# Kernel optimization log

Measured on AMD Instinct MI355X. Metric: run time of the kernel, lower is better.

The kernel has to match this reference:

```python
import jax, jax.numpy as jnp
import numpy as np

PRE_NMS_TOPK = 6000
POST_NMS_TOPK = 1000
NMS_THRESH = 0.7
MIN_SIZE = 16.0
NEG = -1e9  # stand-in for -inf that is safe under autodiff


def setup_inputs() -> dict:
    key = jax.random.key(0)
    k1, k2, k3, k4, k5, k6, k7, k8 = jax.random.split(key, 8)
    B, A = 8, 200000
    N = B * A
    # realistic anchors: centers within a ~1333x800 canvas, sizes 16..256
    cx = jax.random.uniform(k1, (N,), minval=0.0, maxval=1200.0)
    cy = jax.random.uniform(k2, (N,), minval=0.0, maxval=800.0)
    w = jax.random.uniform(k3, (N,), minval=16.0, maxval=256.0)
    h = jax.random.uniform(k4, (N,), minval=16.0, maxval=256.0)
    anchors = jnp.stack([cx - 0.5 * w, cy - 0.5 * h, cx + 0.5 * w, cy + 0.5 * h], axis=1)
    batch_indices = jnp.sort(jax.random.randint(k5, (N,), 0, B)).astype(jnp.int32)
    image_sizes = jax.random.randint(k6, (B, 2), 600, 1334).astype(jnp.int32)  # (H, W)
    objectness_logits = jax.random.normal(k7, (N, 1), dtype=jnp.float32)
    bbox_deltas = jax.random.normal(k8, (N, 4), dtype=jnp.float32) * 0.2
    return {
        'anchors': anchors,
        'batch_indices': batch_indices,
        'image_sizes': image_sizes,
        'objectness_logits': objectness_logits,
        'bbox_deltas': bbox_deltas,
    }


def _nms_one(bx, sc):
    """Greedy NMS on [K,4] boxes / [K] scores; returns POST_NMS_TOPK (idx, ok)."""
    K = bx.shape[0]
    areas = (bx[:, 2] - bx[:, 0]) * (bx[:, 3] - bx[:, 1])
    ar = jnp.arange(K)

    def step(sup, _):
        s = jnp.where(sup, NEG, sc)
        j = jnp.argmax(s)
        ok = s[j] > 0.5 * NEG
        b = bx[j]
        ix1 = jnp.maximum(b[0], bx[:, 0])
        iy1 = jnp.maximum(b[1], bx[:, 1])
        ix2 = jnp.minimum(b[2], bx[:, 2])
        iy2 = jnp.minimum(b[3], bx[:, 3])
        inter = jnp.maximum(ix2 - ix1, 0.0) * jnp.maximum(iy2 - iy1, 0.0)
        iou = inter / (areas + areas[j] - inter + 1e-9)
        sup = sup | (iou > NMS_THRESH) | (ar == j)
        return sup, (j, ok)

    sup0 = sc <= 0.5 * NEG  # padded / invalid entries start suppressed
    _, (idx, ok) = jax.lax.scan(step, sup0, None, length=POST_NMS_TOPK)
    return idx, ok


def reference(anchors, batch_indices, image_sizes, objectness_logits, bbox_deltas):
    B = image_sizes.shape[0]
    N = anchors.shape[0]
    sizes = image_sizes[batch_indices].astype(jnp.float32)  # [N,2] (H,W) per anchor

    # --- box decode ---
    a_w = anchors[:, 2] - anchors[:, 0]
    a_h = anchors[:, 3] - anchors[:, 1]
    a_x = anchors[:, 0] + 0.5 * a_w
    a_y = anchors[:, 1] + 0.5 * a_h
    t_x, t_y = bbox_deltas[:, 0], bbox_deltas[:, 1]
    t_w, t_h = bbox_deltas[:, 2], bbox_deltas[:, 3]
    p_x = a_x + t_x * a_w
    p_y = a_y + t_y * a_h
    p_w = a_w * jnp.exp(jnp.clip(t_w, -10.0, 10.0))
    p_h = a_h * jnp.exp(jnp.clip(t_h, -10.0, 10.0))
    x1 = p_x - 0.5 * p_w
    y1 = p_y - 0.5 * p_h
    x2 = p_x + 0.5 * p_w
    y2 = p_y + 0.5 * p_h

    # --- clip to image ---
    H, W = sizes[:, 0], sizes[:, 1]
    x1 = jnp.clip(x1, 0.0, W - 1.0)
    y1 = jnp.clip(y1, 0.0, H - 1.0)
    x2 = jnp.clip(x2, 0.0, W - 1.0)
    y2 = jnp.clip(y2, 0.0, H - 1.0)
    boxes = jnp.stack([x1, y1, x2, y2], axis=1)  # [N,4]

    # --- min-size filter (as score masking) ---
    valid = ((x2 - x1) >= MIN_SIZE) & ((y2 - y1) >= MIN_SIZE)
    fg = jax.nn.sigmoid(objectness_logits[:, 0])

    # --- per-image top-k over masked scores ---
    img_mask = batch_indices[None, :] == jnp.arange(B, dtype=batch_indices.dtype)[:, None]  # [B,N]
    scores = jnp.where(img_mask & valid[None, :], fg[None, :], NEG)  # [B,N]
    top_scores, top_idx = jax.lax.top_k(scores, PRE_NMS_TOPK)  # [B,PRE]
    top_boxes = boxes[top_idx]  # [B,PRE,4]

    # --- NMS per image ---
    keep_idx, keep_ok = jax.vmap(_nms_one)(top_boxes, top_scores)  # [B,POST]

    sel = jnp.take_along_axis(top_idx, keep_idx, axis=1)  # global anchor indices [B,POST]
    okf = keep_ok[..., None].astype(boxes.dtype)
    props = jnp.take_along_axis(top_boxes, keep_idx[..., None], axis=1) * okf  # [B,POST,4]
    obj = objectness_logits[sel] * okf  # [B,POST,1]
    deltas_out = bbox_deltas[sel] * okf  # [B,POST,4]
    bidx = jnp.where(keep_ok, jnp.arange(B, dtype=jnp.int32)[:, None], -1)  # [B,POST]

    return (props.reshape(-1, 4), bidx.reshape(-1), obj.reshape(-1, 1),
            deltas_out.reshape(-1, 4), keep_ok.reshape(-1))
```

## Files before the change

kernel.cpp:

```cpp
#include <hip/hip_runtime.h>
#include <stdint.h>

#define PRE_K   6000
#define POST_K  1000
#define CAP     8192
#define BINS    1024
#define ROWS    6016
#define CH      94
#define RC_CH   32
#define JSPLIT  4
#define NEGF    -1000000000.0f
#define IOU_EPS 16.0f


__device__ __forceinline__ uint32_t orderf(float f) {
  uint32_t u = __float_as_uint(f);
  return (u & 0x80000000u) ? ~u : (u | 0x80000000u);
}

__device__ __forceinline__ int score_bin(float sc) {
  int bin = (int)floorf((sc + 12.0f) * ((float)BINS / 24.0f));
  return bin < 0 ? 0 : (bin > BINS - 1 ? BINS - 1 : bin);
}

__device__ __forceinline__ int bin_slot(int bin) {
  return ((bin & 15) << 6) | (bin >> 4);
}

__device__ __forceinline__ void decode_box(
    const float* __restrict__ anchors, const float* __restrict__ deltas,
    const int* __restrict__ isz, int n, int b,
    double& x1, double& y1, double& x2, double& y2, bool& valid) {
  double ax1 = (double)anchors[4 * n + 0], ay1 = (double)anchors[4 * n + 1];
  double ax2 = (double)anchors[4 * n + 2], ay2 = (double)anchors[4 * n + 3];
  double aw = ax2 - ax1, ah = ay2 - ay1;
  double acx = ax1 + 0.5 * aw, acy = ay1 + 0.5 * ah;
  double tx = (double)deltas[4 * n + 0], ty = (double)deltas[4 * n + 1];
  double tw = (double)deltas[4 * n + 2], th = (double)deltas[4 * n + 3];
  tw = tw < -10.0 ? -10.0 : (tw > 10.0 ? 10.0 : tw);
  th = th < -10.0 ? -10.0 : (th > 10.0 ? 10.0 : th);
  double px = acx + tx * aw, py = acy + ty * ah;
  double pw = aw * exp(tw), ph = ah * exp(th);
  double H = (double)isz[2 * b + 0], W = (double)isz[2 * b + 1];
  double wm = W - 1.0, hm = H - 1.0;
  x1 = px - 0.5 * pw; y1 = py - 0.5 * ph;
  x2 = px + 0.5 * pw; y2 = py + 0.5 * ph;
  x1 = fmin(fmax(x1, 0.0), wm); x2 = fmin(fmax(x2, 0.0), wm);
  y1 = fmin(fmax(y1, 0.0), hm); y2 = fmin(fmax(y2, 0.0), hm);
  valid = (x2 - x1 >= 16.0) && (y2 - y1 >= 16.0);
}

__device__ __forceinline__ bool iou_exact(const double* __restrict__ tbox,
                                          const double* __restrict__ tarea,
                                          size_t ri, size_t ci) {
  const double* pr = &tbox[ri * 4];
  const double* pc = &tbox[ci * 4];
  double w = fmin(pr[2], pc[2]) - fmax(pr[0], pc[0]); w = w > 0.0 ? w : 0.0;
  double h = fmin(pr[3], pc[3]) - fmax(pr[1], pc[1]); h = h > 0.0 ? h : 0.0;
  double it = w * h;
  return it > 0.7 * (tarea[ri] + tarea[ci] - it + 1e-9);
}


__global__ void k_init(uint32_t* hist, uint32_t* cnt, uint32_t* prank, int B) {
  int i = blockIdx.x * blockDim.x + threadIdx.x;
  if (i < B * BINS) hist[i] = 0u;
  if (i < B) cnt[i] = 0u;
  if (i < B * CAP) prank[i] = 0u;
}

__global__ void __launch_bounds__(256) k_score(const float* __restrict__ anchors,
                                               const int* __restrict__ bix,
                                               const int* __restrict__ isz,
                                               const float* __restrict__ logits,
                                               const float* __restrict__ deltas,
                                               float* __restrict__ scores,
                                               uint32_t* __restrict__ hist, int N) {
  const int SPAN = 4096;
  int start = blockIdx.x * SPAN;
  int end = start + SPAN < N ? start + SPAN : N;
  __shared__ uint32_t lh[2][BINS];
  for (int i = threadIdx.x; i < 2 * BINS; i += 256) ((uint32_t*)lh)[i] = 0u;
  __shared__ int s_b0, s_b1;
  if (threadIdx.x == 0) { s_b0 = bix[start]; s_b1 = bix[end - 1]; }
  __syncthreads();
  int b0 = s_b0, b1 = s_b1;

  for (int n = start + (int)threadIdx.x; n < end; n += 256) {
    int b = bix[n];
    double x1, y1, x2, y2; bool valid;
    decode_box(anchors, deltas, isz, n, b, x1, y1, x2, y2, valid);
    float sc = valid ? logits[n] : NEGF;
    scores[n] = sc;
    if (valid) {
      int bin = score_bin(sc);
      if (b == b0)      atomicAdd(&lh[0][bin], 1u);
      else if (b == b1) atomicAdd(&lh[1][bin], 1u);
      else              atomicAdd(&hist[b * BINS + bin_slot(bin)], 1u);
    }
  }
  __syncthreads();
  for (int bin = threadIdx.x; bin < BINS; bin += 256) {
    uint32_t c0 = lh[0][bin];
    if (c0) atomicAdd(&hist[b0 * BINS + bin_slot(bin)], c0);
    if (b1 != b0) {
      uint32_t c1 = lh[1][bin];
      if (c1) atomicAdd(&hist[b1 * BINS + bin_slot(bin)], c1);
    }
  }
}

__global__ void k_scan(const uint32_t* __restrict__ hist, uint32_t* __restrict__ bstar) {
  __shared__ uint32_t s[BINS];
  __shared__ int bs;
  int b = blockIdx.x, t = threadIdx.x;
  s[t] = hist[b * BINS + bin_slot(t)];
  if (t == 0) bs = 0;
  __syncthreads();
  for (int off = 1; off < BINS; off <<= 1) {
    uint32_t v = (t + off < BINS) ? s[t + off] : 0u;
    __syncthreads();
    s[t] += v;
    __syncthreads();
  }
  if (s[t] >= PRE_K) atomicMax(&bs, t);
  __syncthreads();
  if (t == 0) bstar[b] = (uint32_t)bs;
}

__global__ void __launch_bounds__(1024) k_compact(const float* __restrict__ scores,
                                                  const int* __restrict__ bix,
                                                  const uint32_t* __restrict__ bstar,
                                                  uint32_t* __restrict__ cnt,
                                                  uint64_t* __restrict__ cand, int N) {
  const int SPAN = 8192;
  int start = blockIdx.x * SPAN;
  int end = start + SPAN < N ? start + SPAN : N;
  __shared__ uint32_t lcnt[8], lbase[8];
  if (threadIdx.x < 8) lcnt[threadIdx.x] = 0u;
  __syncthreads();

  bool     predv[8];
  uint64_t keyv[8];
  uint32_t lposv[8];
  int      bv[8];
  int nt = 0;
  for (int base = start; base < end; base += 1024, nt++) {
    int n = base + (int)threadIdx.x;
    bool pred = false; int b = 0; uint64_t key = 0ull; uint32_t lp = 0u;
    if (n < end) {
      float sc = scores[n];
      if (sc > 0.5f * NEGF) {
        b = bix[n];
        if ((uint32_t)score_bin(sc) >= bstar[b]) {
          pred = true;
          key = ((uint64_t)orderf(sc) << 32) | (uint64_t)(uint32_t)(~(uint32_t)n);
          lp = atomicAdd(&lcnt[b], 1u);
        }
      }
    }
    predv[nt] = pred; keyv[nt] = key; lposv[nt] = lp; bv[nt] = b;
  }
  __syncthreads();
  if (threadIdx.x < 8) {
    uint32_t c = lcnt[threadIdx.x];
    lbase[threadIdx.x] = c ? atomicAdd(&cnt[threadIdx.x], c) : 0u;
  }
  __syncthreads();
  for (int k = 0; k < nt; k++) {
    if (predv[k]) {
      uint32_t pos = lbase[bv[k]] + lposv[k];
      if (pos < CAP) cand[(size_t)bv[k] * CAP + pos] = keyv[k];
    }
  }
}

__global__ void __launch_bounds__(256) k_rank(const uint64_t* __restrict__ cand,
                                              const uint32_t* __restrict__ cnt,
                                              uint32_t* __restrict__ prank) {
  int blk = blockIdx.x;
  int js = blk % JSPLIT;
  int ic = (blk / JSPLIT) % 32;
  int b  = blk / (JSPLIT * 32);
  int t = threadIdx.x;
  int C = (int)min(cnt[b], (uint32_t)CAP);
  if (ic * 256 >= C) return;
  const uint64_t* g = cand + (size_t)b * CAP;
  int i = ic * 256 + t;
  uint64_t ki = (i < C) ? g[i] : 0ull;

  int q = (C + JSPLIT - 1) / JSPLIT;
  int j0 = js * q;
  int j1 = j0 + q < C ? j0 + q : C;
  if (j0 >= j1) return;

  __shared__ uint64_t tile[1024];
  int rank = 0;
  for (int base = j0; base < j1; base += 1024) {
#pragma unroll
    for (int u = 0; u < 4; u++) {
      int j = base + u * 256 + t;
      tile[u * 256 + t] = (j < j1) ? g[j] : 0ull;
    }
    __syncthreads();
    int lim = j1 - base < 1024 ? j1 - base : 1024;
    const ulonglong2* t2 = (const ulonglong2*)tile;
    int pairs = lim >> 1;
    int jj = 0;
    for (; jj + 4 <= pairs; jj += 4) {
      ulonglong2 v0 = t2[jj + 0], v1 = t2[jj + 1];
      ulonglong2 v2 = t2[jj + 2], v3 = t2[jj + 3];
      rank += (v0.x > ki) ? 1 : 0; rank += (v0.y > ki) ? 1 : 0;
      rank += (v1.x > ki) ? 1 : 0; rank += (v1.y > ki) ? 1 : 0;
      rank += (v2.x > ki) ? 1 : 0; rank += (v2.y > ki) ? 1 : 0;
      rank += (v3.x > ki) ? 1 : 0; rank += (v3.y > ki) ? 1 : 0;
    }
    for (; jj < pairs; jj++) {
      ulonglong2 v = t2[jj];
      rank += (v.x > ki) ? 1 : 0; rank += (v.y > ki) ? 1 : 0;
    }
    if (lim & 1) rank += (tile[lim - 1] > ki) ? 1 : 0;
    __syncthreads();
  }
  if (i < C && rank) atomicAdd(&prank[b * CAP + i], (uint32_t)rank);
}

__global__ void __launch_bounds__(256) k_place_gather(
    const uint64_t* __restrict__ cand, const uint32_t* __restrict__ cnt,
    const uint32_t* __restrict__ prank,
    const float* __restrict__ anchors, const float* __restrict__ deltas,
    const int* __restrict__ isz,
    double* __restrict__ tbox, double* __restrict__ tarea,
    float4* __restrict__ tboxf, float* __restrict__ tareaf,
    int* __restrict__ top_n, int* __restrict__ Cnum, int B) {
  int idx = blockIdx.x * blockDim.x + threadIdx.x;
  if (idx >= B * CAP) return;
  int b = idx / CAP, i = idx % CAP;
  int C = (int)min(cnt[b], (uint32_t)CAP);
  if (i == 0) Cnum[b] = C < PRE_K ? C : PRE_K;
  if (i >= C) return;
  uint32_t rank = prank[idx];
  if (rank >= PRE_K) return;
  int n = (int)(~(uint32_t)(cand[idx] & 0xFFFFFFFFull));
  double x1, y1, x2, y2; bool valid;
  decode_box(anchors, deltas, isz, n, b, x1, y1, x2, y2, valid);
  size_t row = (size_t)b * ROWS + rank;
  tbox[row * 4 + 0] = x1;
  tbox[row * 4 + 1] = y1;
  tbox[row * 4 + 2] = x2;
  tbox[row * 4 + 3] = y2;
  double ar = (x2 - x1) * (y2 - y1);
  tarea[row] = ar;
  tboxf[row] = make_float4((float)x1, (float)y1, (float)x2, (float)y2);
  tareaf[row] = (float)ar;
  top_n[b * PRE_K + rank] = n;
}

__global__ void __launch_bounds__(64) k_iou_mat(const float4* __restrict__ tboxf,
                                                const float* __restrict__ tareaf,
                                                const double* __restrict__ tbox,
                                                const double* __restrict__ tarea,
                                                const int* __restrict__ Cnum,
                                                uint32_t* __restrict__ maskT) {
  int blk = blockIdx.x;
  int k  = blk % (RC_CH + 1);
  int cc = (blk / (RC_CH + 1)) % CH;
  int b  = blk / ((RC_CH + 1) * CH);
  int rc = (k == RC_CH) ? cc : k;
  if (k < RC_CH && cc <= rc) return;
  int C = Cnum[b];
  if (rc * 64 >= C || cc * 64 >= C) return;
  int lane = threadIdx.x;
  size_t bb = (size_t)b * ROWS;

  float4 cb4 = tboxf[bb + (size_t)cc * 64 + lane];
  float  sca = 0.7f * tareaf[bb + (size_t)cc * 64 + lane];
  __shared__ float4 rbx[64];
  __shared__ float  rsa[64];
  rbx[lane] = tboxf[bb + (size_t)rc * 64 + lane];
  rsa[lane] = 0.7f * tareaf[bb + (size_t)rc * 64 + lane];
  __syncthreads();

  bool isdiag = (rc == cc);
  uint32_t res0 = 0u, res1 = 0u;

  for (int i = 0; i < 64; i++) {
    float4 r4 = rbx[i];
    float sra = rsa[i];
    float iw = fminf(r4.z, cb4.z) - fmaxf(r4.x, cb4.x);
    float ih = fminf(r4.w, cb4.w) - fmaxf(r4.y, cb4.y);
    iw = fmaxf(iw, 0.0f); ih = fmaxf(ih, 0.0f);
    float inter = iw * ih;
    float diff = fmaf(1.7f, inter, -(sra + sca));
    bool gt = isdiag ? (lane > i) : true;
    unsigned long long sup   = __ballot(gt && (diff >  IOU_EPS));
    unsigned long long loose = __ballot(gt && (diff > -IOU_EPS));
    unsigned long long border = loose & ~sup;
    if (border) {
      bool mine = (border >> lane) & 1ull;
      bool ex = false;
      if (mine)
        ex = iou_exact(tbox, tarea, bb + (size_t)rc * 64 + i,
                       bb + (size_t)cc * 64 + lane);
      sup |= __ballot(ex);
    }
    if (lane == i) { res0 = (uint32_t)sup; res1 = (uint32_t)(sup >> 32); }
  }
  uint2* seg = (uint2*)(maskT + (((size_t)b * CH + cc) * ROWS + (size_t)rc * 64) * 2);
  seg[lane] = make_uint2(res0, res1);
}

__global__ void __launch_bounds__(256) k_nms_reduce(const uint32_t* __restrict__ maskT,
                                                    const float4* __restrict__ tboxf,
                                                    const float* __restrict__ tareaf,
                                                    const double* __restrict__ tbox,
                                                    const double* __restrict__ tarea,
                                                    const int* __restrict__ Cnum,
                                                    int* __restrict__ keep,
                                                    int* __restrict__ kept_count) {
  int b = blockIdx.x, t = threadIdx.x;
  int wave = t >> 6, lane = t & 63;
  int C = Cnum[b];
  const uint32_t* M = maskT + (size_t)b * CH * ROWS * 2;
  size_t bb = (size_t)b * ROWS;

  __shared__ uint32_t s_f[2][2];
  __shared__ uint32_t kept_lo[POST_K];
  __shared__ uint32_t kept_hi[POST_K];
  __shared__ uint64_t s_kept;
  if (t < 4) ((uint32_t*)s_f)[t] = 0u;

  uint32_t d0 = 0u, d1 = 0u;
  if (wave == 0) {
    const uint32_t* rp = M + (size_t)lane * 2;
    d0 = rp[0]; d1 = rp[1];
  }
  __syncthreads();

  int nkept = 0, nlo = 0, nhi = 0;
  for (int c = 0; c < CH; c++) {
    int base = c * 64;
    if (base >= C) break;
    int cbuf = c & 1;
    if (t == 0) { s_f[cbuf ^ 1][0] = 0u; s_f[cbuf ^ 1][1] = 0u; }

    uint32_t f0 = 0u, f1 = 0u;
    for (int k2 = t; k2 < nlo; k2 += 256) {
      const uint32_t* rp = M + ((size_t)c * ROWS + kept_lo[k2]) * 2;
      f0 |= rp[0]; f1 |= rp[1];
    }
    if (nhi > 0) {
      float4 cb4 = tboxf[bb + base + lane];
      float  sca = 0.7f * tareaf[bb + base + lane];
      for (int k2 = wave; k2 < nhi; k2 += 4) {
        int r = (int)kept_hi[k2];
        float4 r4 = tboxf[bb + r];
        float sra = 0.7f * tareaf[bb + r];
        float iw = fminf(r4.z, cb4.z) - fmaxf(r4.x, cb4.x);
        float ih = fminf(r4.w, cb4.w) - fmaxf(r4.y, cb4.y);
        iw = fmaxf(iw, 0.0f); ih = fmaxf(ih, 0.0f);
        float inter = iw * ih;
        float diff = fmaf(1.7f, inter, -(sra + sca));
        unsigned long long sup   = __ballot(diff >  IOU_EPS);
        unsigned long long loose = __ballot(diff > -IOU_EPS);
        unsigned long long border = loose & ~sup;
        if (border) {
          bool mine = (border >> lane) & 1ull;
          bool ex = false;
          if (mine) ex = iou_exact(tbox, tarea, bb + r, bb + base + lane);
          sup |= __ballot(ex);
        }
        f0 |= (uint32_t)sup; f1 |= (uint32_t)(sup >> 32);
      }
    }
#pragma unroll
    for (int off = 32; off > 0; off >>= 1) {
      f0 |= (uint32_t)__shfl_xor((int)f0, off, 64);
      f1 |= (uint32_t)__shfl_xor((int)f1, off, 64);
    }
    if (lane == 0 && (f0 | f1)) {
      atomicOr(&s_f[cbuf][0], f0);
      atomicOr(&s_f[cbuf][1], f1);
    }
    __syncthreads();

    if (wave == 0) {
      uint64_t sup = (uint64_t)s_f[cbuf][0] | ((uint64_t)s_f[cbuf][1] << 32);
      int rem = C - base;
      if (rem < 64) sup |= ~((1ull << rem) - 1ull);
      uint64_t diag = (uint64_t)d0 | ((uint64_t)d1 << 32);
      int cn = (c + 1 < CH) ? c + 1 : c;
      const uint32_t* rpn = M + ((size_t)cn * ROWS + (size_t)cn * 64 + lane) * 2;
      uint32_t pn0 = rpn[0], pn1 = rpn[1];

      uint64_t keptMask = 0ull;
      uint64_t alive = ~sup;
      uint64_t m = alive;
      while (m) {
        int i = __builtin_ctzll(m);
        keptMask |= 1ull << i;
        uint64_t d = (uint64_t)__shfl((long long)diag, i, 64);
        sup |= d | (1ull << i);
        m = alive & ~sup;
      }
      int allowed = POST_K - nkept;
      int pc = __popcll(keptMask);
      while (pc > allowed) {
        keptMask &= ~(1ull << (63 - __builtin_clzll(keptMask)));
        pc--;
      }
      if (lane == 0) s_kept = keptMask;
      if ((keptMask >> lane) & 1ull) {
        int pfx = __popcll(keptMask & ((1ull << lane) - 1ull));
        keep[b * POST_K + nkept + pfx] = base + lane;
        if (c < RC_CH) kept_lo[nlo + pfx] = (uint32_t)(base + lane);
        else           kept_hi[nhi + pfx] = (uint32_t)(base + lane);
      }
      d0 = pn0; d1 = pn1;
    }
    __syncthreads();

    int pc = __popcll(s_kept);
    nkept += pc;
    if (c < RC_CH) nlo += pc; else nhi += pc;
    if (nkept >= POST_K) break;
  }
  if (t == 0) kept_count[b] = nkept;
}

__global__ void k_output(const int* __restrict__ keep,
                         const int* __restrict__ kept_count,
                         const int* __restrict__ top_n,
                         const double* __restrict__ tbox,
                         const float* __restrict__ logits,
                         const float* __restrict__ deltas,
                         float* __restrict__ out, int B) {
  int idx = blockIdx.x * blockDim.x + threadIdx.x;
  int M = B * POST_K;
  if (idx >= M) return;
  int b = idx / POST_K, s = idx % POST_K;
  float p0 = 0.f, p1 = 0.f, p2 = 0.f, p3 = 0.f;
  float ob = 0.f, d0 = 0.f, d1 = 0.f, d2 = 0.f, d3 = 0.f;
  float bi = -1.0f, okv = 0.0f;
  if (s < kept_count[b]) {
    int j = keep[b * POST_K + s];
    int n = top_n[b * PRE_K + j];
    const double* p = &tbox[((size_t)b * ROWS + j) * 4];
    p0 = (float)p[0]; p1 = (float)p[1]; p2 = (float)p[2]; p3 = (float)p[3];
    ob = logits[n];
    d0 = deltas[4 * n + 0]; d1 = deltas[4 * n + 1];
    d2 = deltas[4 * n + 2]; d3 = deltas[4 * n + 3];
    bi = (float)b; okv = 1.0f;
  }
  out[idx * 4 + 0] = p0;
  out[idx * 4 + 1] = p1;
  out[idx * 4 + 2] = p2;
  out[idx * 4 + 3] = p3;
  out[4 * M + idx] = bi;
  out[5 * M + idx] = ob;
  out[6 * M + idx * 4 + 0] = d0;
  out[6 * M + idx * 4 + 1] = d1;
  out[6 * M + idx * 4 + 2] = d2;
  out[6 * M + idx * 4 + 3] = d3;
  out[10 * M + idx] = okv;
}


extern "C" void kernel_launch(void* const* d_in, const int* in_sizes, int n_in,
                              void* d_out, int out_size, void* d_ws, size_t ws_size,
                              hipStream_t stream) {
  const float* anchors = (const float*)d_in[0];
  const int*   bix     = (const int*)d_in[1];
  const int*   isz     = (const int*)d_in[2];
  const float* logits  = (const float*)d_in[3];
  const float* deltas  = (const float*)d_in[4];
  float* out = (float*)d_out;

  int N = in_sizes[1];
  int B = in_sizes[2] / 2;

  uintptr_t p = (uintptr_t)d_ws;
  double*   tbox   = (double*)p;    p += (size_t)B * ROWS * 4 * sizeof(double);
  double*   tarea  = (double*)p;    p += (size_t)B * ROWS * sizeof(double);
  uint64_t* cand   = (uint64_t*)p;  p += (size_t)B * CAP * sizeof(uint64_t);
  float*    scores = (float*)p;     p += (size_t)N * sizeof(float);
  uint32_t* hist   = (uint32_t*)p;  p += (size_t)B * BINS * sizeof(uint32_t);
  uint32_t* prank  = (uint32_t*)p;  p += (size_t)B * CAP * sizeof(uint32_t);
  int*      top_n    = (int*)p;     p += (size_t)B * PRE_K * sizeof(int);
  int*      keep     = (int*)p;     p += (size_t)B * POST_K * sizeof(int);
  uint32_t* cnt      = (uint32_t*)p; p += (size_t)B * sizeof(uint32_t);
  uint32_t* bstar    = (uint32_t*)p; p += (size_t)B * sizeof(uint32_t);
  int*      Cnum     = (int*)p;      p += (size_t)B * sizeof(int);
  int*      kept_cnt = (int*)p;      p += (size_t)B * sizeof(int);
  p = (p + 255) & ~(uintptr_t)255;
  uint32_t* maskT    = (uint32_t*)p; p += (size_t)B * CH * ROWS * 2 * sizeof(uint32_t);
  float4*   tboxf  = (float4*)scores;
  float*    tareaf = (float*)(scores + (size_t)B * ROWS * 4);
  (void)ws_size; (void)n_in; (void)out_size;

  int initN = B * CAP;
  k_init<<<(initN + 255) / 256, 256, 0, stream>>>(hist, cnt, prank, B);
  k_score<<<(N + 4095) / 4096, 256, 0, stream>>>(anchors, bix, isz, logits, deltas,
                                                 scores, hist, N);
  k_scan<<<B, BINS, 0, stream>>>(hist, bstar);
  k_compact<<<(N + 8191) / 8192, 1024, 0, stream>>>(scores, bix, bstar, cnt, cand, N);
  k_rank<<<B * 32 * JSPLIT, 256, 0, stream>>>(cand, cnt, prank);
  k_place_gather<<<(B * CAP + 255) / 256, 256, 0, stream>>>(cand, cnt, prank,
                                                            anchors, deltas, isz,
                                                            tbox, tarea, tboxf,
                                                            tareaf, top_n, Cnum, B);
  k_iou_mat<<<B * CH * (RC_CH + 1), 64, 0, stream>>>(tboxf, tareaf, tbox, tarea,
                                                     Cnum, maskT);
  k_nms_reduce<<<B, 256, 0, stream>>>(maskT, tboxf, tareaf, tbox, tarea, Cnum,
                                      keep, kept_cnt);
  k_output<<<(B * POST_K + 255) / 256, 256, 0, stream>>>(keep, kept_cnt, top_n,
                                                         tbox, logits, deltas,
                                                         out, B);
}
```

Before: 354.9 us.

## Fuse scan into compact, output into NMS, and drop rank atomics

Removes the init, scan and output kernels. The histogram threshold scan is recomputed inside each compact block for its one or two images, and the output gather runs at the end of the NMS reduce kernel. Rank partials are now written per j-split slice without atomics and summed in place_gather, which removes the need to zero prank, so init becomes a single memset of hist and cnt. JSPLIT doubles to 8. Launch overhead drops, but every compact block repeats a 1024-bin scan, and the output stage now runs on only B blocks.

```diff
diff --git a/kernel.cpp b/kernel.cpp
--- a/kernel.cpp
+++ b/kernel.cpp
@@ -8,7 +8,7 @@
 #define ROWS    6016
 #define CH      94
 #define RC_CH   32
-#define JSPLIT  4
+#define JSPLIT  8
 #define NEGF    -1000000000.0f
 #define IOU_EPS 16.0f
 
@@ -62,13 +62,6 @@
 }
 
 
-__global__ void k_init(uint32_t* hist, uint32_t* cnt, uint32_t* prank, int B) {
-  int i = blockIdx.x * blockDim.x + threadIdx.x;
-  if (i < B * BINS) hist[i] = 0u;
-  if (i < B) cnt[i] = 0u;
-  if (i < B * CAP) prank[i] = 0u;
-}
-
 __global__ void __launch_bounds__(256) k_score(const float* __restrict__ anchors,
                                                const int* __restrict__ bix,
                                                const int* __restrict__ isz,
@@ -110,35 +103,42 @@
   }
 }
 
-__global__ void k_scan(const uint32_t* __restrict__ hist, uint32_t* __restrict__ bstar) {
-  __shared__ uint32_t s[BINS];
-  __shared__ int bs;
-  int b = blockIdx.x, t = threadIdx.x;
-  s[t] = hist[b * BINS + bin_slot(t)];
-  if (t == 0) bs = 0;
-  __syncthreads();
-  for (int off = 1; off < BINS; off <<= 1) {
-    uint32_t v = (t + off < BINS) ? s[t + off] : 0u;
-    __syncthreads();
-    s[t] += v;
-    __syncthreads();
-  }
-  if (s[t] >= PRE_K) atomicMax(&bs, t);
-  __syncthreads();
-  if (t == 0) bstar[b] = (uint32_t)bs;
-}
-
 __global__ void __launch_bounds__(1024) k_compact(const float* __restrict__ scores,
                                                   const int* __restrict__ bix,
-                                                  const uint32_t* __restrict__ bstar,
+                                                  const uint32_t* __restrict__ hist,
                                                   uint32_t* __restrict__ cnt,
                                                   uint64_t* __restrict__ cand, int N) {
   const int SPAN = 8192;
   int start = blockIdx.x * SPAN;
   int end = start + SPAN < N ? start + SPAN : N;
+  int t = threadIdx.x;
+  __shared__ int s_b0, s_b1;
+  __shared__ uint32_t sh[BINS];
+  __shared__ int s_bs;
   __shared__ uint32_t lcnt[8], lbase[8];
-  if (threadIdx.x < 8) lcnt[threadIdx.x] = 0u;
-  __syncthreads();
+  if (t == 0) { s_b0 = bix[start]; s_b1 = bix[end - 1]; }
+  if (t < 8) lcnt[t] = 0u;
+  __syncthreads();
+  int b0 = s_b0, b1 = s_b1;
+
+  uint32_t bs0 = 0, bs1 = 0;
+  for (int pass = 0; pass < 2; pass++) {
+    int b = pass == 0 ? b0 : b1;
+    if (pass == 1 && b1 == b0) { bs1 = bs0; break; }
+    if (t < BINS) sh[t] = hist[b * BINS + bin_slot(t)];
+    if (t == 0) s_bs = 0;
+    __syncthreads();
+    for (int off = 1; off < BINS; off <<= 1) {
+      uint32_t v = (t < BINS && t + off < BINS) ? sh[t + off] : 0u;
+      __syncthreads();
+      if (t < BINS) sh[t] += v;
+      __syncthreads();
+    }
+    if (t < BINS && sh[t] >= PRE_K) atomicMax(&s_bs, t);
+    __syncthreads();
+    if (pass == 0) bs0 = (uint32_t)s_bs; else bs1 = (uint32_t)s_bs;
+    __syncthreads();
+  }
 
   bool     predv[8];
   uint64_t keyv[8];
@@ -146,13 +146,14 @@
   int      bv[8];
   int nt = 0;
   for (int base = start; base < end; base += 1024, nt++) {
-    int n = base + (int)threadIdx.x;
+    int n = base + t;
     bool pred = false; int b = 0; uint64_t key = 0ull; uint32_t lp = 0u;
     if (n < end) {
       float sc = scores[n];
       if (sc > 0.5f * NEGF) {
         b = bix[n];
-        if ((uint32_t)score_bin(sc) >= bstar[b]) {
+        uint32_t bs = (b == b0) ? bs0 : bs1;
+        if ((uint32_t)score_bin(sc) >= bs) {
           pred = true;
           key = ((uint64_t)orderf(sc) << 32) | (uint64_t)(uint32_t)(~(uint32_t)n);
           lp = atomicAdd(&lcnt[b], 1u);
@@ -162,9 +163,9 @@
     predv[nt] = pred; keyv[nt] = key; lposv[nt] = lp; bv[nt] = b;
   }
   __syncthreads();
-  if (threadIdx.x < 8) {
-    uint32_t c = lcnt[threadIdx.x];
-    lbase[threadIdx.x] = c ? atomicAdd(&cnt[threadIdx.x], c) : 0u;
+  if (t < 8) {
+    uint32_t c = lcnt[t];
+    lbase[t] = c ? atomicAdd(&cnt[t], c) : 0u;
   }
   __syncthreads();
   for (int k = 0; k < nt; k++) {
@@ -192,7 +193,6 @@
   int q = (C + JSPLIT - 1) / JSPLIT;
   int j0 = js * q;
   int j1 = j0 + q < C ? j0 + q : C;
-  if (j0 >= j1) return;
 
   __shared__ uint64_t tile[1024];
   int rank = 0;
@@ -222,7 +222,7 @@
     if (lim & 1) rank += (tile[lim - 1] > ki) ? 1 : 0;
     __syncthreads();
   }
-  if (i < C && rank) atomicAdd(&prank[b * CAP + i], (uint32_t)rank);
+  if (i < C) prank[((size_t)b * JSPLIT + js) * CAP + i] = (uint32_t)rank;
 }
 
 __global__ void __launch_bounds__(256) k_place_gather(
@@ -239,7 +239,10 @@
   int C = (int)min(cnt[b], (uint32_t)CAP);
   if (i == 0) Cnum[b] = C < PRE_K ? C : PRE_K;
   if (i >= C) return;
-  uint32_t rank = prank[idx];
+  uint32_t rank = 0;
+#pragma unroll
+  for (int js = 0; js < JSPLIT; js++)
+    rank += prank[((size_t)b * JSPLIT + js) * CAP + i];
   if (rank >= PRE_K) return;
   int n = (int)(~(uint32_t)(cand[idx] & 0xFFFFFFFFull));
   double x1, y1, x2, y2; bool valid;
@@ -316,8 +319,10 @@
                                                     const double* __restrict__ tbox,
                                                     const double* __restrict__ tarea,
                                                     const int* __restrict__ Cnum,
-                                                    int* __restrict__ keep,
-                                                    int* __restrict__ kept_count) {
+                                                    const int* __restrict__ top_n,
+                                                    const float* __restrict__ logits,
+                                                    const float* __restrict__ deltas,
+                                                    float* __restrict__ out, int B) {
   int b = blockIdx.x, t = threadIdx.x;
   int wave = t >> 6, lane = t & 63;
   int C = Cnum[b];
@@ -412,9 +417,9 @@
       if (lane == 0) s_kept = keptMask;
       if ((keptMask >> lane) & 1ull) {
         int pfx = __popcll(keptMask & ((1ull << lane) - 1ull));
-        keep[b * POST_K + nkept + pfx] = base + lane;
-        if (c < RC_CH) kept_lo[nlo + pfx] = (uint32_t)(base + lane);
-        else           kept_hi[nhi + pfx] = (uint32_t)(base + lane);
+        int row = base + lane;
+        if (c < RC_CH) kept_lo[nlo + pfx] = (uint32_t)row;
+        else           kept_hi[nhi + pfx] = (uint32_t)row;
       }
       d0 = pn0; d1 = pn1;
     }
@@ -425,44 +430,36 @@
     if (c < RC_CH) nlo += pc; else nhi += pc;
     if (nkept >= POST_K) break;
   }
-  if (t == 0) kept_count[b] = nkept;
-}
-
-__global__ void k_output(const int* __restrict__ keep,
-                         const int* __restrict__ kept_count,
-                         const int* __restrict__ top_n,
-                         const double* __restrict__ tbox,
-                         const float* __restrict__ logits,
-                         const float* __restrict__ deltas,
-                         float* __restrict__ out, int B) {
-  int idx = blockIdx.x * blockDim.x + threadIdx.x;
-  int M = B * POST_K;
-  if (idx >= M) return;
-  int b = idx / POST_K, s = idx % POST_K;
-  float p0 = 0.f, p1 = 0.f, p2 = 0.f, p3 = 0.f;
-  float ob = 0.f, d0 = 0.f, d1 = 0.f, d2 = 0.f, d3 = 0.f;
-  float bi = -1.0f, okv = 0.0f;
-  if (s < kept_count[b]) {
-    int j = keep[b * POST_K + s];
-    int n = top_n[b * PRE_K + j];
-    const double* p = &tbox[((size_t)b * ROWS + j) * 4];
-    p0 = (float)p[0]; p1 = (float)p[1]; p2 = (float)p[2]; p3 = (float)p[3];
-    ob = logits[n];
-    d0 = deltas[4 * n + 0]; d1 = deltas[4 * n + 1];
-    d2 = deltas[4 * n + 2]; d3 = deltas[4 * n + 3];
-    bi = (float)b; okv = 1.0f;
-  }
-  out[idx * 4 + 0] = p0;
-  out[idx * 4 + 1] = p1;
-  out[idx * 4 + 2] = p2;
-  out[idx * 4 + 3] = p3;
-  out[4 * M + idx] = bi;
-  out[5 * M + idx] = ob;
-  out[6 * M + idx * 4 + 0] = d0;
-  out[6 * M + idx * 4 + 1] = d1;
-  out[6 * M + idx * 4 + 2] = d2;
-  out[6 * M + idx * 4 + 3] = d3;
-  out[10 * M + idx] = okv;
+
+  __syncthreads();
+  int M_out = B * POST_K;
+  for (int s2 = t; s2 < POST_K; s2 += 256) {
+    float p0 = 0.f, p1 = 0.f, p2 = 0.f, p3 = 0.f;
+    float ob = 0.f, d0f = 0.f, d1f = 0.f, d2f = 0.f, d3f = 0.f;
+    float bi = -1.0f, okv = 0.0f;
+    if (s2 < nkept) {
+      int j = (s2 < nlo) ? (int)kept_lo[s2] : (int)kept_hi[s2 - nlo];
+      int n = top_n[b * PRE_K + j];
+      const double* p = &tbox[(bb + j) * 4];
+      p0 = (float)p[0]; p1 = (float)p[1]; p2 = (float)p[2]; p3 = (float)p[3];
+      ob = logits[n];
+      d0f = deltas[4 * n + 0]; d1f = deltas[4 * n + 1];
+      d2f = deltas[4 * n + 2]; d3f = deltas[4 * n + 3];
+      bi = (float)b; okv = 1.0f;
+    }
+    int idx = b * POST_K + s2;
+    out[idx * 4 + 0] = p0;
+    out[idx * 4 + 1] = p1;
+    out[idx * 4 + 2] = p2;
+    out[idx * 4 + 3] = p3;
+    out[4 * M_out + idx] = bi;
+    out[5 * M_out + idx] = ob;
+    out[6 * M_out + idx * 4 + 0] = d0f;
+    out[6 * M_out + idx * 4 + 1] = d1f;
+    out[6 * M_out + idx * 4 + 2] = d2f;
+    out[6 * M_out + idx * 4 + 3] = d3f;
+    out[10 * M_out + idx] = okv;
+  }
 }
 
 
@@ -485,25 +482,20 @@
   uint64_t* cand   = (uint64_t*)p;  p += (size_t)B * CAP * sizeof(uint64_t);
   float*    scores = (float*)p;     p += (size_t)N * sizeof(float);
   uint32_t* hist   = (uint32_t*)p;  p += (size_t)B * BINS * sizeof(uint32_t);
-  uint32_t* prank  = (uint32_t*)p;  p += (size_t)B * CAP * sizeof(uint32_t);
+  uint32_t* cnt    = (uint32_t*)p;  p += (size_t)B * sizeof(uint32_t);
+  uint32_t* prank  = (uint32_t*)p;  p += (size_t)B * JSPLIT * CAP * sizeof(uint32_t);
   int*      top_n    = (int*)p;     p += (size_t)B * PRE_K * sizeof(int);
-  int*      keep     = (int*)p;     p += (size_t)B * POST_K * sizeof(int);
-  uint32_t* cnt      = (uint32_t*)p; p += (size_t)B * sizeof(uint32_t);
-  uint32_t* bstar    = (uint32_t*)p; p += (size_t)B * sizeof(uint32_t);
   int*      Cnum     = (int*)p;      p += (size_t)B * sizeof(int);
-  int*      kept_cnt = (int*)p;      p += (size_t)B * sizeof(int);
   p = (p + 255) & ~(uintptr_t)255;
   uint32_t* maskT    = (uint32_t*)p; p += (size_t)B * CH * ROWS * 2 * sizeof(uint32_t);
   float4*   tboxf  = (float4*)scores;
   float*    tareaf = (float*)(scores + (size_t)B * ROWS * 4);
   (void)ws_size; (void)n_in; (void)out_size;
 
-  int initN = B * CAP;
-  k_init<<<(initN + 255) / 256, 256, 0, stream>>>(hist, cnt, prank, B);
+  hipMemsetAsync(hist, 0, (size_t)(B * BINS + B) * sizeof(uint32_t), stream);
   k_score<<<(N + 4095) / 4096, 256, 0, stream>>>(anchors, bix, isz, logits, deltas,
                                                  scores, hist, N);
-  k_scan<<<B, BINS, 0, stream>>>(hist, bstar);
-  k_compact<<<(N + 8191) / 8192, 1024, 0, stream>>>(scores, bix, bstar, cnt, cand, N);
+  k_compact<<<(N + 8191) / 8192, 1024, 0, stream>>>(scores, bix, hist, cnt, cand, N);
   k_rank<<<B * 32 * JSPLIT, 256, 0, stream>>>(cand, cnt, prank);
   k_place_gather<<<(B * CAP + 255) / 256, 256, 0, stream>>>(cand, cnt, prank,
                                                             anchors, deltas, isz,
@@ -512,8 +504,5 @@
   k_iou_mat<<<B * CH * (RC_CH + 1), 64, 0, stream>>>(tboxf, tareaf, tbox, tarea,
                                                      Cnum, maskT);
   k_nms_reduce<<<B, 256, 0, stream>>>(maskT, tboxf, tareaf, tbox, tarea, Cnum,
-                                      keep, kept_cnt);
-  k_output<<<(B * POST_K + 255) / 256, 256, 0, stream>>>(keep, kept_cnt, top_n,
-                                                         tbox, logits, deltas,
-                                                         out, B);
-}
+                                      top_n, logits, deltas, out, B);
+}
```

Result: no change. 353.4 us (-0.4%).
